# Kernel tuning notes

Hardware: AMD Instinct MI355X
Metric: run time of the kernel (lower is better)

The kernel has to match this reference:

```python
import jax, jax.numpy as jnp
import numpy as np

N_NODES = 100000
N_EDGES = 1250000
D_FEAT = 64


def setup_inputs() -> dict:
    key = jax.random.key(0)
    kx, ke = jax.random.split(key)
    x = jax.random.normal(kx, (N_NODES, D_FEAT), dtype=jnp.float32)
    edge_index = jax.random.randint(ke, (2, N_EDGES), 0, N_NODES, dtype=jnp.int64)
    return {"x": x, "edge_index": edge_index}


def _aggregate(x, src, dst, num_nodes):
    # out[i] = sum_{e: dst[e]==i} x[src[e]]  (identity message, 'add' aggr)
    return jax.ops.segment_sum(x[src], dst, num_segments=num_nodes)


def reference(x, edge_index):
    num_nodes = x.shape[0]
    src, dst = edge_index[0], edge_index[1]  # PyG source_to_target flow
    h = _aggregate(x, src, dst, num_nodes)   # conv1
    h = jax.nn.relu(h)
    h = _aggregate(h, src, dst, num_nodes)   # conv2
    return h
```

## Files before the change

kernel.cpp:

```cpp
#include <hip/hip_runtime.h>
#include <hip/hip_bf16.h>


#define N_FEAT    64
#define BIN_SHIFT 7
#define BIN_NODES 128
#define CAPBIN    2048
#define NB_H      784
#define NSCAN     1024
#define GSTRIDE   16
#define TILE      4096
#define EPT       16
#define NPTR      (BIN_NODES + 1)
#define SRCSH     14

typedef unsigned int u32;
typedef unsigned short u16;
typedef __attribute__((ext_vector_type(8))) unsigned short u16x8;
typedef __attribute__((ext_vector_type(4))) unsigned int u32x4;
typedef __attribute__((ext_vector_type(2))) float f32x2;

__device__ inline u16 f2bf(float f) {
    u32 u = __builtin_bit_cast(u32, f);
    return (u16)((u + 0x7FFFu + ((u >> 16) & 1u)) >> 16);
}

__global__ __launch_bounds__(256) void convert_kernel(
    const float* __restrict__ xf, u16* __restrict__ xb, int n_elems)
{
    int i = ((int)blockIdx.x * 256 + (int)threadIdx.x) * 8;
    if (i < n_elems) {
        float4 a = *(const float4*)(xf + i);
        float4 b = *(const float4*)(xf + i + 4);
        u16x8 r;
        r[0]=f2bf(a.x); r[1]=f2bf(a.y); r[2]=f2bf(a.z); r[3]=f2bf(a.w);
        r[4]=f2bf(b.x); r[5]=f2bf(b.y); r[6]=f2bf(b.z); r[7]=f2bf(b.w);
        *(u16x8*)(xb + i) = r;
    }
}

__global__ __launch_bounds__(256) void partition_kernel(
    const int* __restrict__ src, const int* __restrict__ dst,
    u32* __restrict__ gcur,
    u32* __restrict__ cbdata,
    int n_edges, int n_bins)
{
    __shared__ u32 hist[NSCAN];
    __shared__ u32 starts[NSCAN];
    __shared__ u32 lpos[NSCAN];
    __shared__ u32 wcur[NB_H];
    __shared__ u32 sortbuf[TILE];
    __shared__ u16 binid[TILE];
    __shared__ u32 wsum[4];

    const int tid   = threadIdx.x;
    const int tbase = (int)blockIdx.x * TILE;
    const int tend  = min(tbase + TILE, n_edges);

    for (int i = tid; i < NSCAN; i += 256) { hist[i] = 0; lpos[i] = 0; }
    __syncthreads();

    u32 breg[EPT];
    u32 preg[EPT];
    #pragma unroll
    for (int k = 0; k < EPT; ++k) {
        int e = tbase + tid + k * 256;
        breg[k] = ~0u;
        if (e < tend) {
            int d = dst[e];
            int s = src[e];
            breg[k] = (u32)d >> BIN_SHIFT;
            preg[k] = ((u32)(d & (BIN_NODES - 1)) << 17) | (u32)s;
            atomicAdd(&hist[breg[k]], 1u);
        }
    }
    __syncthreads();

    {
        const int b0 = tid * 4;
        u32 h0 = hist[b0], h1 = hist[b0+1], h2 = hist[b0+2], h3 = hist[b0+3];
        u32 s  = h0 + h1 + h2 + h3;
        u32 inc = s;
        #pragma unroll
        for (int d = 1; d < 64; d <<= 1) {
            u32 o = __shfl_up(inc, d);
            if ((tid & 63) >= d) inc += o;
        }
        if ((tid & 63) == 63) wsum[tid >> 6] = inc;
        __syncthreads();
        u32 woff = 0;
        #pragma unroll
        for (int k = 0; k < 4; ++k) if (k < (tid >> 6)) woff += wsum[k];
        u32 excl = woff + inc - s;
        starts[b0]   = excl;
        starts[b0+1] = excl + h0;
        starts[b0+2] = excl + h0 + h1;
        starts[b0+3] = excl + h0 + h1 + h2;
    }
    __syncthreads();

    const int rot = (int)(((u32)blockIdx.x * 193u) % (u32)n_bins);
    for (int i = tid; i < n_bins; i += 256) {
        int b = i + rot; if (b >= n_bins) b -= n_bins;
        u32 h = hist[b];
        if (h) wcur[b] = atomicAdd(&gcur[b * GSTRIDE], h);
    }
    __syncthreads();

    #pragma unroll
    for (int k = 0; k < EPT; ++k) {
        if (breg[k] != ~0u) {
            u32 b   = breg[k];
            u32 pos = starts[b] + atomicAdd(&lpos[b], 1u);
            sortbuf[pos] = preg[k];
            binid[pos]   = (u16)b;
        }
    }
    __syncthreads();

    const int cnt = tend - tbase;
    for (int j = tid; j < cnt; j += 256) {
        u32 b   = binid[j];
        u32 rel = wcur[b] + ((u32)j - starts[b]);
        if (rel < CAPBIN)
            cbdata[(size_t)b * CAPBIN + rel] = sortbuf[j];
    }
}

__global__ __launch_bounds__(256) void bin_sort_kernel(
    u32* __restrict__ cbdata,
    const u32* __restrict__ gcur,
    u32* __restrict__ nodeptr,
    int n_bins)
{
    __shared__ u32 hist[NSCAN];
    __shared__ u32 starts[NSCAN];
    __shared__ u32 lpos[NSCAN];
    __shared__ u32 sl[CAPBIN];
    __shared__ u32 wsum[4];

    const int tid = threadIdx.x;
    const int bin = blockIdx.x;
    if (bin >= n_bins) return;

    for (int i = tid; i < NSCAN; i += 256) { hist[i] = 0; lpos[i] = 0; }
    __syncthreads();

    int cnt = (int)gcur[bin * GSTRIDE];
    if (cnt > CAPBIN) cnt = CAPBIN;
    u32* bd = cbdata + (size_t)bin * CAPBIN;

    for (int j = tid; j < cnt; j += 256) {
        u32 p = bd[j];
        u32 key = ((p >> 17) << 3) | ((p & 0x1FFFFu) >> SRCSH);
        atomicAdd(&hist[key], 1u);
    }
    __syncthreads();

    {
        const int b0 = tid * 4;
        u32 h0 = hist[b0], h1 = hist[b0+1], h2 = hist[b0+2], h3 = hist[b0+3];
        u32 s  = h0 + h1 + h2 + h3;
        u32 inc = s;
        #pragma unroll
        for (int d = 1; d < 64; d <<= 1) {
            u32 o = __shfl_up(inc, d);
            if ((tid & 63) >= d) inc += o;
        }
        if ((tid & 63) == 63) wsum[tid >> 6] = inc;
        __syncthreads();
        u32 woff = 0;
        #pragma unroll
        for (int k = 0; k < 4; ++k) if (k < (tid >> 6)) woff += wsum[k];
        u32 excl = woff + inc - s;
        starts[b0]   = excl;
        starts[b0+1] = excl + h0;
        starts[b0+2] = excl + h0 + h1;
        starts[b0+3] = excl + h0 + h1 + h2;
    }
    __syncthreads();

    for (int j = tid; j < cnt; j += 256) {
        u32 p   = bd[j];
        u32 key = ((p >> 17) << 3) | ((p & 0x1FFFFu) >> SRCSH);
        u32 pos = starts[key] + atomicAdd(&lpos[key], 1u);
        sl[pos] = p & 0x1FFFFu;
    }
    __syncthreads();

    const u32 base = (u32)bin * CAPBIN;
    for (int j = tid; j < cnt; j += 256)
        bd[j] = sl[j];
    if (tid < BIN_NODES)
        nodeptr[(size_t)bin * NPTR + tid] = base + starts[tid << 3];
    if (tid == 0)
        nodeptr[(size_t)bin * NPTR + BIN_NODES] = base + (u32)cnt;
}

__global__ __launch_bounds__(256) void aggregate_kernel(
    const u16* __restrict__ xin,
    const u32* __restrict__ csorted,
    const u32* __restrict__ nodeptr,
    u16* __restrict__ out_bf,
    float* __restrict__ out_f,
    int n_nodes, int pass)
{
    const int tid  = threadIdx.x;

    const int w    = tid >> 6;
    const int lane = tid & 63;
    const int grp  = lane >> 3;
    const int sub  = lane & 7;
    const char* xc = (const char*)xin;

    const int nl   = w * 8 + grp;
    const int node = (int)blockIdx.x * 32 + nl;
    const int bin  = node >> BIN_SHIFT;
    const int nid  = node & (BIN_NODES - 1);

    const int s0  = (int)nodeptr[(size_t)bin * NPTR + nid];
    const int s1  = (int)nodeptr[(size_t)bin * NPTR + nid + 1];

    f32x2 a0={0.f,0.f}, a1={0.f,0.f}, a2={0.f,0.f}, a3={0.f,0.f};

    int jb = s0;
    for (; jb + 8 <= s1; jb += 8) {
        u32 myid = csorted[jb + sub];
        #pragma unroll
        for (int k = 0; k < 8; ++k) {
            u32 s = (u32)__shfl((int)myid, (lane & 56) + k, 64);
            u32x4 v = *(const u32x4*)(xc + ((size_t)s << 7) + (sub << 4));
            a0 += (f32x2){ __builtin_bit_cast(float, v[0] << 16),
                           __builtin_bit_cast(float, v[0] & 0xFFFF0000u) };
            a1 += (f32x2){ __builtin_bit_cast(float, v[1] << 16),
                           __builtin_bit_cast(float, v[1] & 0xFFFF0000u) };
            a2 += (f32x2){ __builtin_bit_cast(float, v[2] << 16),
                           __builtin_bit_cast(float, v[2] & 0xFFFF0000u) };
            a3 += (f32x2){ __builtin_bit_cast(float, v[3] << 16),
                           __builtin_bit_cast(float, v[3] & 0xFFFF0000u) };
        }
    }
    if (jb < s1) {
        u32 myid = 0;
        if (jb + sub < s1) myid = csorted[jb + sub];
        const int m = s1 - jb;
        #pragma unroll 1
        for (int k = 0; k < m; ++k) {
            u32 s = (u32)__shfl((int)myid, (lane & 56) + k, 64);
            u32x4 v = *(const u32x4*)(xc + ((size_t)s << 7) + (sub << 4));
            a0 += (f32x2){ __builtin_bit_cast(float, v[0] << 16),
                           __builtin_bit_cast(float, v[0] & 0xFFFF0000u) };
            a1 += (f32x2){ __builtin_bit_cast(float, v[1] << 16),
                           __builtin_bit_cast(float, v[1] & 0xFFFF0000u) };
            a2 += (f32x2){ __builtin_bit_cast(float, v[2] << 16),
                           __builtin_bit_cast(float, v[2] & 0xFFFF0000u) };
            a3 += (f32x2){ __builtin_bit_cast(float, v[3] << 16),
                           __builtin_bit_cast(float, v[3] & 0xFFFF0000u) };
        }
    }

    if (node < n_nodes) {
        if (pass == 0) {
            u16x8 o;
            o[0]=f2bf(fmaxf(a0.x,0.f)); o[1]=f2bf(fmaxf(a0.y,0.f));
            o[2]=f2bf(fmaxf(a1.x,0.f)); o[3]=f2bf(fmaxf(a1.y,0.f));
            o[4]=f2bf(fmaxf(a2.x,0.f)); o[5]=f2bf(fmaxf(a2.y,0.f));
            o[6]=f2bf(fmaxf(a3.x,0.f)); o[7]=f2bf(fmaxf(a3.y,0.f));
            *(u16x8*)(out_bf + (size_t)node * N_FEAT + sub * 8) = o;
        } else {
            float* dp = out_f + (size_t)node * N_FEAT + sub * 8;
            *(float4*)dp       = (float4){a0.x, a0.y, a1.x, a1.y};
            *(float4*)(dp + 4) = (float4){a2.x, a2.y, a3.x, a3.y};
        }
    }
}

extern "C" void kernel_launch(void* const* d_in, const int* in_sizes, int n_in,
                              void* d_out, int out_size, void* d_ws, size_t ws_size,
                              hipStream_t stream) {
    const float* x          = (const float*)d_in[0];
    const int*   edge_index = (const int*)d_in[1];

    const int n_edges = in_sizes[1] / 2;
    const int* src = edge_index;
    const int* dst = edge_index + n_edges;

    const int n_nodes = out_size / N_FEAT;
    const int n_bins  = (n_nodes + BIN_NODES - 1) >> BIN_SHIFT;
    float* out = (float*)d_out;

    const size_t xb_bytes    = (size_t)out_size * sizeof(u16);
    const size_t hb_bytes    = (size_t)out_size * sizeof(u16);
    const size_t cb_bytes    = (size_t)n_bins * CAPBIN * sizeof(u32);
    const size_t np_bytes    = (size_t)n_bins * NPTR * sizeof(u32);
    const size_t gcur_bytes  = (size_t)NB_H * GSTRIDE * sizeof(u32);

    char* w = (char*)d_ws;
    u16* xb      = (u16*)w;              w += xb_bytes;
    u16* hb      = (u16*)w;              w += hb_bytes;
    u32* cbdata  = (u32*)w;              w += cb_bytes;
    u32* nodeptr = (u32*)w;              w += np_bytes;
    u32* gcur    = (u32*)w;

    hipMemsetAsync(gcur, 0, gcur_bytes, stream);

    const int conv_blocks = (out_size / 8 + 255) / 256;
    convert_kernel<<<conv_blocks, 256, 0, stream>>>(x, xb, out_size);

    const int part_blocks = (n_edges + TILE - 1) / TILE;
    partition_kernel<<<part_blocks, 256, 0, stream>>>(
        src, dst, gcur, cbdata, n_edges, n_bins);

    bin_sort_kernel<<<n_bins, 256, 0, stream>>>(cbdata, gcur, nodeptr, n_bins);

    const int agg_blocks = (n_nodes + 31) / 32;
    aggregate_kernel<<<agg_blocks, 256, 0, stream>>>(xb, cbdata, nodeptr, hb, nullptr, n_nodes, 0);
    aggregate_kernel<<<agg_blocks, 256, 0, stream>>>(hb, cbdata, nodeptr, nullptr, out, n_nodes, 1);
}
```

Before: 163.6 us.

## Fuse first aggregation into bin sort kernel and widen partition blocks

```diff
diff --git a/kernel.cpp b/kernel.cpp
--- a/kernel.cpp
+++ b/kernel.cpp
@@ -10,7 +10,8 @@
 #define NSCAN     1024
 #define GSTRIDE   16
 #define TILE      4096
-#define EPT       16
+#define PTHREADS  512
+#define EPT       8
 #define NPTR      (BIN_NODES + 1)
 #define SRCSH     14
 
@@ -39,7 +40,7 @@
     }
 }
 
-__global__ __launch_bounds__(256) void partition_kernel(
+__global__ __launch_bounds__(PTHREADS) void partition_kernel(
     const int* __restrict__ src, const int* __restrict__ dst,
     u32* __restrict__ gcur,
     u32* __restrict__ cbdata,
@@ -51,20 +52,20 @@
     __shared__ u32 wcur[NB_H];
     __shared__ u32 sortbuf[TILE];
     __shared__ u16 binid[TILE];
-    __shared__ u32 wsum[4];
+    __shared__ u32 wsum[PTHREADS / 64];
 
     const int tid   = threadIdx.x;
     const int tbase = (int)blockIdx.x * TILE;
     const int tend  = min(tbase + TILE, n_edges);
 
-    for (int i = tid; i < NSCAN; i += 256) { hist[i] = 0; lpos[i] = 0; }
+    for (int i = tid; i < NSCAN; i += PTHREADS) { hist[i] = 0; lpos[i] = 0; }
     __syncthreads();
 
     u32 breg[EPT];
     u32 preg[EPT];
     #pragma unroll
     for (int k = 0; k < EPT; ++k) {
-        int e = tbase + tid + k * 256;
+        int e = tbase + tid + k * PTHREADS;
         breg[k] = ~0u;
         if (e < tend) {
             int d = dst[e];
@@ -77,9 +78,9 @@
     __syncthreads();
 
     {
-        const int b0 = tid * 4;
-        u32 h0 = hist[b0], h1 = hist[b0+1], h2 = hist[b0+2], h3 = hist[b0+3];
-        u32 s  = h0 + h1 + h2 + h3;
+        const int b0 = tid * 2;
+        u32 h0 = hist[b0], h1 = hist[b0 + 1];
+        u32 s  = h0 + h1;
         u32 inc = s;
         #pragma unroll
         for (int d = 1; d < 64; d <<= 1) {
@@ -90,17 +91,15 @@
         __syncthreads();
         u32 woff = 0;
         #pragma unroll
-        for (int k = 0; k < 4; ++k) if (k < (tid >> 6)) woff += wsum[k];
+        for (int k = 0; k < PTHREADS / 64; ++k) if (k < (tid >> 6)) woff += wsum[k];
         u32 excl = woff + inc - s;
-        starts[b0]   = excl;
-        starts[b0+1] = excl + h0;
-        starts[b0+2] = excl + h0 + h1;
-        starts[b0+3] = excl + h0 + h1 + h2;
+        starts[b0]     = excl;
+        starts[b0 + 1] = excl + h0;
     }
     __syncthreads();
 
     const int rot = (int)(((u32)blockIdx.x * 193u) % (u32)n_bins);
-    for (int i = tid; i < n_bins; i += 256) {
+    for (int i = tid; i < n_bins; i += PTHREADS) {
         int b = i + rot; if (b >= n_bins) b -= n_bins;
         u32 h = hist[b];
         if (h) wcur[b] = atomicAdd(&gcur[b * GSTRIDE], h);
@@ -119,7 +118,7 @@
     __syncthreads();
 
     const int cnt = tend - tbase;
-    for (int j = tid; j < cnt; j += 256) {
+    for (int j = tid; j < cnt; j += PTHREADS) {
         u32 b   = binid[j];
         u32 rel = wcur[b] + ((u32)j - starts[b]);
         if (rel < CAPBIN)
@@ -127,11 +126,13 @@
     }
 }
 
-__global__ __launch_bounds__(256) void bin_sort_kernel(
+__global__ __launch_bounds__(256) void sort_aggregate_kernel(
+    const u16* __restrict__ xin,
     u32* __restrict__ cbdata,
     const u32* __restrict__ gcur,
     u32* __restrict__ nodeptr,
-    int n_bins)
+    u16* __restrict__ out_bf,
+    int n_nodes, int n_bins)
 {
     __shared__ u32 hist[NSCAN];
     __shared__ u32 starts[NSCAN];
@@ -195,15 +196,69 @@
         nodeptr[(size_t)bin * NPTR + tid] = base + starts[tid << 3];
     if (tid == 0)
         nodeptr[(size_t)bin * NPTR + BIN_NODES] = base + (u32)cnt;
+
+    const int w    = tid >> 6;
+    const int lane = tid & 63;
+    const int grp  = lane >> 3;
+    const int sub  = lane & 7;
+    const char* xc = (const char*)xin;
+
+    #pragma unroll 1
+    for (int rep = 0; rep < 4; ++rep) {
+        const int nid  = w * 8 + grp + rep * 32;
+        const int node = bin * BIN_NODES + nid;
+        const int s0 = (int)starts[nid << 3];
+        const int s1 = (nid < BIN_NODES - 1) ? (int)starts[(nid + 1) << 3] : cnt;
+
+        f32x2 a0={0.f,0.f}, a1={0.f,0.f}, a2={0.f,0.f}, a3={0.f,0.f};
+
+        int jb = s0;
+        for (; jb + 8 <= s1; jb += 8) {
+            #pragma unroll
+            for (int k = 0; k < 8; ++k) {
+                u32 s = sl[jb + k];
+                u32x4 v = *(const u32x4*)(xc + ((size_t)s << 7) + (sub << 4));
+                a0 += (f32x2){ __builtin_bit_cast(float, v[0] << 16),
+                               __builtin_bit_cast(float, v[0] & 0xFFFF0000u) };
+                a1 += (f32x2){ __builtin_bit_cast(float, v[1] << 16),
+                               __builtin_bit_cast(float, v[1] & 0xFFFF0000u) };
+                a2 += (f32x2){ __builtin_bit_cast(float, v[2] << 16),
+                               __builtin_bit_cast(float, v[2] & 0xFFFF0000u) };
+                a3 += (f32x2){ __builtin_bit_cast(float, v[3] << 16),
+                               __builtin_bit_cast(float, v[3] & 0xFFFF0000u) };
+            }
+        }
+        #pragma unroll 1
+        for (; jb < s1; ++jb) {
+            u32 s = sl[jb];
+            u32x4 v = *(const u32x4*)(xc + ((size_t)s << 7) + (sub << 4));
+            a0 += (f32x2){ __builtin_bit_cast(float, v[0] << 16),
+                           __builtin_bit_cast(float, v[0] & 0xFFFF0000u) };
+            a1 += (f32x2){ __builtin_bit_cast(float, v[1] << 16),
+                           __builtin_bit_cast(float, v[1] & 0xFFFF0000u) };
+            a2 += (f32x2){ __builtin_bit_cast(float, v[2] << 16),
+                           __builtin_bit_cast(float, v[2] & 0xFFFF0000u) };
+            a3 += (f32x2){ __builtin_bit_cast(float, v[3] << 16),
+                           __builtin_bit_cast(float, v[3] & 0xFFFF0000u) };
+        }
+
+        if (node < n_nodes) {
+            u16x8 o;
+            o[0]=f2bf(fmaxf(a0.x,0.f)); o[1]=f2bf(fmaxf(a0.y,0.f));
+            o[2]=f2bf(fmaxf(a1.x,0.f)); o[3]=f2bf(fmaxf(a1.y,0.f));
+            o[4]=f2bf(fmaxf(a2.x,0.f)); o[5]=f2bf(fmaxf(a2.y,0.f));
+            o[6]=f2bf(fmaxf(a3.x,0.f)); o[7]=f2bf(fmaxf(a3.y,0.f));
+            *(u16x8*)(out_bf + (size_t)node * N_FEAT + sub * 8) = o;
+        }
+    }
 }
 
 __global__ __launch_bounds__(256) void aggregate_kernel(
     const u16* __restrict__ xin,
     const u32* __restrict__ csorted,
     const u32* __restrict__ nodeptr,
-    u16* __restrict__ out_bf,
     float* __restrict__ out_f,
-    int n_nodes, int pass)
+    int n_nodes)
 {
     const int tid  = threadIdx.x;
 
@@ -260,18 +315,9 @@
     }
 
     if (node < n_nodes) {
-        if (pass == 0) {
-            u16x8 o;
-            o[0]=f2bf(fmaxf(a0.x,0.f)); o[1]=f2bf(fmaxf(a0.y,0.f));
-            o[2]=f2bf(fmaxf(a1.x,0.f)); o[3]=f2bf(fmaxf(a1.y,0.f));
-            o[4]=f2bf(fmaxf(a2.x,0.f)); o[5]=f2bf(fmaxf(a2.y,0.f));
-            o[6]=f2bf(fmaxf(a3.x,0.f)); o[7]=f2bf(fmaxf(a3.y,0.f));
-            *(u16x8*)(out_bf + (size_t)node * N_FEAT + sub * 8) = o;
-        } else {
-            float* dp = out_f + (size_t)node * N_FEAT + sub * 8;
-            *(float4*)dp       = (float4){a0.x, a0.y, a1.x, a1.y};
-            *(float4*)(dp + 4) = (float4){a2.x, a2.y, a3.x, a3.y};
-        }
+        float* dp = out_f + (size_t)node * N_FEAT + sub * 8;
+        *(float4*)dp       = (float4){a0.x, a0.y, a1.x, a1.y};
+        *(float4*)(dp + 4) = (float4){a2.x, a2.y, a3.x, a3.y};
     }
 }
 
@@ -308,12 +354,12 @@
     convert_kernel<<<conv_blocks, 256, 0, stream>>>(x, xb, out_size);
 
     const int part_blocks = (n_edges + TILE - 1) / TILE;
-    partition_kernel<<<part_blocks, 256, 0, stream>>>(
+    partition_kernel<<<part_blocks, PTHREADS, 0, stream>>>(
         src, dst, gcur, cbdata, n_edges, n_bins);
 
-    bin_sort_kernel<<<n_bins, 256, 0, stream>>>(cbdata, gcur, nodeptr, n_bins);
+    sort_aggregate_kernel<<<n_bins, 256, 0, stream>>>(
+        xb, cbdata, gcur, nodeptr, hb, n_nodes, n_bins);
 
     const int agg_blocks = (n_nodes + 31) / 32;
-    aggregate_kernel<<<agg_blocks, 256, 0, stream>>>(xb, cbdata, nodeptr, hb, nullptr, n_nodes, 0);
-    aggregate_kernel<<<agg_blocks, 256, 0, stream>>>(hb, cbdata, nodeptr, nullptr, out, n_nodes, 1);
-}
+    aggregate_kernel<<<agg_blocks, 256, 0, stream>>>(hb, cbdata, nodeptr, out, n_nodes);
+}
```

After: 162.1 us. No clear change (-0.9%).
